# Kernel optimization log

Hardware: AMD Instinct MI355X
Metric: run time of the kernel (lower is better)

## Reference

```python
import jax, jax.numpy as jnp
import numpy as np

EPS = 1e-5
SLOPE = 0.2
K = 20
B, N = 8, 2048

def _lrelu(x):
    return jnp.where(x >= 0, x, SLOPE * x)

def _bn(x, g, b, m, v, axis):
    # eval-mode batchnorm with running stats
    shape = [1] * x.ndim
    shape[axis] = -1
    g, b, m, v = (t.reshape(shape) for t in (g, b, m, v))
    return g * (x - m) * jax.lax.rsqrt(v + EPS) + b

def _knn(x, k):
    # x: (B, C, N) -> neighbor indices (B, N, k) by largest negative sq dist
    xx = jnp.sum(x * x, axis=1)                      # (B, N)
    inner = jnp.einsum('bcn,bcm->bnm', x, x)         # (B, N, N)
    pd = 2.0 * inner - xx[:, :, None] - xx[:, None, :]
    return jax.lax.top_k(pd, k)[1]

def _graph_feature(x, k):
    # x: (B, C, N) -> (B, 2C, N, k) edge features [nbr - center, center]
    idx = _knn(x, k)                                  # (B, N, k)
    xt = jnp.transpose(x, (0, 2, 1))                  # (B, N, C)
    nbr = xt[jnp.arange(x.shape[0])[:, None, None], idx]  # (B, N, k, C)
    center = xt[:, :, None, :]
    f = jnp.concatenate([nbr - center, jnp.broadcast_to(center, nbr.shape)], axis=-1)
    return jnp.transpose(f, (0, 3, 1, 2))

def _edge_block(x, W, g, b, m, v):
    f = _graph_feature(x, K)                          # (B, 2C, N, k)
    h = jnp.einsum('oc,bcnk->bonk', W, f)             # 1x1 conv
    return jnp.max(_lrelu(_bn(h, g, b, m, v, 1)), axis=-1)

def _forward(x, W1, bn1_g, bn1_b, bn1_m, bn1_v, W2, bn2_g, bn2_b, bn2_m, bn2_v, W3, bn3_g, bn3_b, bn3_m, bn3_v, W4, bn4_g, bn4_b, bn4_m, bn4_v, l1_w, l1_b, bn5_g, bn5_b, bn5_m, bn5_v, l2_w, l2_b, bn6_g, bn6_b, bn6_m, bn6_v, l3_w, l3_b):
    xc = jnp.transpose(x, (0, 2, 1))                  # (B, 3, N)
    x1 = _edge_block(xc, W1, bn1_g, bn1_b, bn1_m, bn1_v)   # (B, 64, N)
    x2 = _edge_block(x1, W2, bn2_g, bn2_b, bn2_m, bn2_v)   # (B, 64, N)
    x3 = _edge_block(x2, W3, bn3_g, bn3_b, bn3_m, bn3_v)   # (B, 128, N)
    h = jnp.concatenate([x1, x2, x3], axis=1)         # (B, 256, N)
    h = _lrelu(_bn(jnp.einsum('oc,bcn->bon', W4, h), bn4_g, bn4_b, bn4_m, bn4_v, 1))
    h = jnp.max(h, axis=-1)                           # (B, 1024)
    h = _lrelu(_bn(h @ l1_w.T + l1_b, bn5_g, bn5_b, bn5_m, bn5_v, 1))
    h = _lrelu(_bn(h @ l2_w.T + l2_b, bn6_g, bn6_b, bn6_m, bn6_v, 1))
    return h @ l3_w.T + l3_b                          # (B, 2)

def setup_inputs() -> dict:
    key = jax.random.key(0)
    ks = iter(jax.random.split(key, 64))
    def rn(shape, s=1.0):
        return jax.random.normal(next(ks), shape, jnp.float32) * s
    def add_bn(inp, prefix, c):
        inp[prefix + '_g'] = jax.random.uniform(next(ks), (c,), jnp.float32, 0.5, 1.5)
        inp[prefix + '_b'] = rn((c,), 0.1)
        inp[prefix + '_m'] = rn((c,), 0.1)
        inp[prefix + '_v'] = jax.random.uniform(next(ks), (c,), jnp.float32, 0.5, 1.5)
    inp = {'x': rn((B, N, 3))}
    inp['W1'] = rn((64, 6), 0.3); add_bn(inp, 'bn1', 64)
    inp['W2'] = rn((64, 128), 0.1); add_bn(inp, 'bn2', 64)
    inp['W3'] = rn((128, 128), 0.1); add_bn(inp, 'bn3', 128)
    inp['W4'] = rn((1024, 256), 0.08); add_bn(inp, 'bn4', 1024)
    inp['l1_w'] = rn((512, 1024), 0.03); inp['l1_b'] = rn((512,), 0.01); add_bn(inp, 'bn5', 512)
    inp['l2_w'] = rn((256, 512), 0.05); inp['l2_b'] = rn((256,), 0.01); add_bn(inp, 'bn6', 256)
    inp['l3_w'] = rn((2, 256), 0.06); inp['l3_b'] = rn((2,), 0.01)
    return inp

def reference(x, W1, bn1_g, bn1_b, bn1_m, bn1_v, W2, bn2_g, bn2_b, bn2_m, bn2_v, W3, bn3_g, bn3_b, bn3_m, bn3_v, W4, bn4_g, bn4_b, bn4_m, bn4_v, l1_w, l1_b, bn5_g, bn5_b, bn5_m, bn5_v, l2_w, l2_b, bn6_g, bn6_b, bn6_m, bn6_v, l3_w, l3_b):
    return _forward(x, W1, bn1_g, bn1_b, bn1_m, bn1_v, W2, bn2_g, bn2_b, bn2_m, bn2_v, W3, bn3_g, bn3_b, bn3_m, bn3_v, W4, bn4_g, bn4_b, bn4_m, bn4_v, l1_w, l1_b, bn5_g, bn5_b, bn5_m, bn5_v, l2_w, l2_b, bn6_g, bn6_b, bn6_m, bn6_v, l3_w, l3_b)
```

## Files before the change

kernel.cpp:

```cpp
#include <hip/hip_runtime.h>
#include <math.h>

#define NN 2048
#define KK 20
#define EPSF 1e-5f

__device__ __forceinline__ float lrelu(float v){ return v >= 0.f ? v : 0.2f*v; }

__device__ __forceinline__ void topk20_insert(float d, int idc, float (&v)[KK], int (&id)[KK]){
#pragma unroll
  for (int j = KK-1; j >= 1; --j){
    bool cjm1 = d > v[j-1];
    bool cj   = d > v[j];
    float nv = cjm1 ? v[j-1] : (cj ? d   : v[j]);
    int   ni = cjm1 ? id[j-1] : (cj ? idc : id[j]);
    v[j] = nv; id[j] = ni;
  }
  if (d > v[0]) { v[0] = d; id[0] = idc; }
}

__global__ void k_prep1(const float* __restrict__ x, const float* __restrict__ W1,
                        float* __restrict__ Y, float* __restrict__ T, float* __restrict__ SQ){
  __shared__ float wa[64][3], wd[64][3];
  int t = threadIdx.x;
  if (t < 64){
#pragma unroll
    for (int c=0;c<3;c++){
      float a = W1[t*6+c], b2 = W1[t*6+3+c];
      wa[t][c] = a; wd[t][c] = b2 - a;
    }
  }
  __syncthreads();
  int gid = blockIdx.x*256 + t;
  int b = gid >> 11, n = gid & (NN-1);
  float px = x[gid*3+0], py = x[gid*3+1], pz = x[gid*3+2];
  SQ[gid] = px*px + py*py + pz*pz;
  float* yb = Y + ((size_t)b*128)*NN + n;
  float* tb = T + ((size_t)b*128)*NN + n;
#pragma unroll 8
  for (int o=0;o<64;o++){
    yb[(size_t)o*NN] = wa[o][0]*px + wa[o][1]*py + wa[o][2]*pz;
    tb[(size_t)o*NN] = wd[o][0]*px + wd[o][1]*py + wd[o][2]*pz;
  }
}

__global__ __launch_bounds__(256) void k_knn3(const float* __restrict__ x, const float* __restrict__ SQ,
                                              int* __restrict__ IDX){
  __shared__ __align__(16) unsigned char smem[30720];
  float* cd = (float*)smem;
  float* VL = (float*)smem;
  unsigned short* IL = (unsigned short*)(smem + 20480);
  int t = threadIdx.x;
  int b = blockIdx.x >> 6;
  int n_base = (blockIdx.x & 63) * 32;
  int ql = t & 31, sp = t >> 5;
  int n = n_base + ql;
  int gq = b*NN + n;
  float qx = x[gq*3], qy = x[gq*3+1], qz = x[gq*3+2];
  float qs = SQ[gq];
  float v[KK]; int id[KK];
#pragma unroll
  for (int i=0;i<KK;i++){ v[i] = -INFINITY; id[i] = 0; }
  int mlo = sp * 16;
  for (int tile=0; tile<16; ++tile){
    int m0 = tile * 128;
    __syncthreads();
#pragma unroll
    for (int i=0;i<2;i++){
      int f2 = t + i*256;
      int m = f2 >> 2, ch = f2 & 3;
      int gm = b*NN + m0 + m;
      cd[f2] = (ch < 3) ? x[gm*3 + ch] : SQ[gm];
    }
    __syncthreads();
    for (int j=mlo; j<mlo+16; ++j){
      float4 c4 = *(const float4*)&cd[j*4];
      float d = 2.f*(qx*c4.x + qy*c4.y + qz*c4.z) - qs - c4.w;
      if (d > v[KK-1]) topk20_insert(d, m0 + j, v, id);
    }
  }
  __syncthreads();
#pragma unroll
  for (int k2=0;k2<KK;k2++){
    VL[(ql*8+sp)*KK + k2] = v[k2];
    IL[(ql*8+sp)*KK + k2] = (unsigned short)id[k2];
  }
  __syncthreads();
  if (t < 32){
    float hv[8]; int hi_[8]; int hp[8];
#pragma unroll
    for (int s=0;s<8;s++){ hp[s]=0; hv[s]=VL[(t*8+s)*KK]; hi_[s]=(int)IL[(t*8+s)*KK]; }
    int nq = n_base + t;
    for (int r=0;r<KK;r++){
      float bv = hv[0]; int bi = hi_[0]; int bs = 0;
#pragma unroll
      for (int s=1;s<8;s++){
        bool win = (hv[s] > bv) || ((hv[s] == bv) && (hi_[s] < bi));
        bv = win ? hv[s] : bv; bi = win ? hi_[s] : bi; bs = win ? s : bs;
      }
      IDX[((size_t)b*KK + r)*NN + nq] = bi;
#pragma unroll
      for (int s=0;s<8;s++){
        if (s == bs){
          int np = hp[s] + 1; hp[s] = np;
          bool ok = np < KK;
          hv[s]  = ok ? VL[(t*8+s)*KK + np] : -INFINITY;
          hi_[s] = ok ? (int)IL[(t*8+s)*KK + np] : 0x7FFFFFFF;
        }
      }
    }
  }
}

__global__ void k_sqnorm(const float* __restrict__ X, float* __restrict__ SQ){
  int gid = blockIdx.x*256 + threadIdx.x;
  int b = gid >> 11, n = gid & (NN-1);
  const float* xb = X + (size_t)b*256*NN;
  float s = 0.f;
#pragma unroll
  for (int c=0;c<64;c++){ float vv = xb[(size_t)c*NN + n]; s += vv*vv; }
  SQ[gid] = s;
}

__global__ __launch_bounds__(256) void k_knn64(const float* __restrict__ X, const float* __restrict__ SQ,
                                               int* __restrict__ IDX){
  __shared__ __align__(16) unsigned char smem[35328];
  float* cd = (float*)smem;
  float* cs = (float*)(smem + 34816);
  float* VL = (float*)smem;
  unsigned short* IL = (unsigned short*)(smem + 20480);
  int t = threadIdx.x;
  int b = blockIdx.x >> 6;
  int n_base = (blockIdx.x & 63) * 32;
  int ql = t & 31, sp = t >> 5;
  int n = n_base + ql;
  const float* xb = X + (size_t)b*256*NN;
  float q[64];
#pragma unroll
  for (int c=0;c<64;c++) q[c] = xb[(size_t)c*NN + n];
  float qs = SQ[b*NN + n];
  float v[KK]; int id[KK];
#pragma unroll
  for (int i=0;i<KK;i++){ v[i]=-INFINITY; id[i]=0; }
  int mlo = sp * 16;
  for (int tile=0; tile<16; ++tile){
    int m0 = tile*128;
    __syncthreads();
#pragma unroll
    for (int i=0;i<32;i++){
      int flat = i*256 + t;
      int c = flat >> 7, m = flat & 127;
      cd[m*68 + c] = xb[(size_t)c*NN + m0 + m];
    }
    if (t < 128) cs[t] = SQ[b*NN + m0 + t];
    __syncthreads();
    for (int j=mlo; j<mlo+16; ++j){
      const float* crow = cd + j*68;
      float d = 0.f;
#pragma unroll
      for (int c=0;c<64;c+=4){
        float4 c4 = *(const float4*)&crow[c];
        d += q[c]*c4.x + q[c+1]*c4.y + q[c+2]*c4.z + q[c+3]*c4.w;
      }
      d = 2.f*d - qs - cs[j];
      if (d > v[KK-1]) topk20_insert(d, m0 + j, v, id);
    }
  }
  __syncthreads();
#pragma unroll
  for (int k2=0;k2<KK;k2++){
    VL[(ql*8+sp)*KK + k2] = v[k2];
    IL[(ql*8+sp)*KK + k2] = (unsigned short)id[k2];
  }
  __syncthreads();
  if (t < 32){
    float hv[8]; int hi_[8]; int hp[8];
#pragma unroll
    for (int s=0;s<8;s++){ hp[s]=0; hv[s]=VL[(t*8+s)*KK]; hi_[s]=(int)IL[(t*8+s)*KK]; }
    int nq = n_base + t;
    for (int r=0;r<KK;r++){
      float bv = hv[0]; int bi = hi_[0]; int bs = 0;
#pragma unroll
      for (int s=1;s<8;s++){
        bool win = (hv[s] > bv) || ((hv[s] == bv) && (hi_[s] < bi));
        bv = win ? hv[s] : bv; bi = win ? hi_[s] : bi; bs = win ? s : bs;
      }
      IDX[((size_t)b*KK + r)*NN + nq] = bi;
#pragma unroll
      for (int s=0;s<8;s++){
        if (s == bs){
          int np = hp[s] + 1; hp[s] = np;
          bool ok = np < KK;
          hv[s]  = ok ? VL[(t*8+s)*KK + np] : -INFINITY;
          hi_[s] = ok ? (int)IL[(t*8+s)*KK + np] : 0x7FFFFFFF;
        }
      }
    }
  }
}

__global__ __launch_bounds__(256) void k_edge_apply(const float* __restrict__ Y, const float* __restrict__ T,
                             const int* __restrict__ IDX,
                             const float* __restrict__ g, const float* __restrict__ be,
                             const float* __restrict__ mu, const float* __restrict__ va,
                             float* __restrict__ OUT, int c_off){
  int t = threadIdx.x;
  int nl = t & 127, oh = t >> 7;
  int n = blockIdx.x*128 + nl;
  int b = blockIdx.z;
  int o0 = blockIdx.y*32 + oh*16;
  int idx[KK];
#pragma unroll
  for (int k2=0;k2<KK;k2++) idx[k2] = IDX[((size_t)b*KK + k2)*NN + n];
  for (int oo=0;oo<16;oo++){
    int o = o0 + oo;
    const float* yrow = Y + ((size_t)b*128 + o)*NN;
    float M = -INFINITY;
#pragma unroll
    for (int k2=0;k2<KK;k2++) M = fmaxf(M, yrow[idx[k2]]);
    float s = g[o] * rsqrtf(va[o] + EPSF);
    float val = s*(M + T[((size_t)b*128 + o)*NN + n] - mu[o]) + be[o];
    OUT[((size_t)b*256 + c_off + o)*NN + n] = lrelu(val);
  }
}

template<int O>
__global__ __launch_bounds__(256) void k_yt_gemm(const float* __restrict__ X, const float* __restrict__ W,
                                                 float* __restrict__ Y, float* __restrict__ T){
  __shared__ __align__(16) float wa[O][64];
  __shared__ __align__(16) float wd[O][64];
  int t = threadIdx.x;
  for (int i=t; i<O*64; i+=256){
    int o = i >> 6, c = i & 63;
    float a = W[o*128 + c];
    wa[o][c] = a;
    wd[o][c] = W[o*128 + 64 + c] - a;
  }
  __syncthreads();
  int half = t >> 7, ln = t & 127;
  int gid = blockIdx.x*128 + ln;
  int b = gid >> 11, n = gid & (NN-1);
  const float* xb = X + (size_t)b*256*NN;
  float q[64];
#pragma unroll
  for (int c=0;c<64;c++) q[c] = xb[(size_t)c*NN + n];
  int o0 = half * (O/2);
  for (int o=o0; o<o0+O/2; ++o){
    float ay=0.f, at=0.f;
#pragma unroll
    for (int c=0;c<64;c+=4){
      float4 a4 = *(const float4*)&wa[o][c];
      float4 d4 = *(const float4*)&wd[o][c];
      ay += a4.x*q[c] + a4.y*q[c+1] + a4.z*q[c+2] + a4.w*q[c+3];
      at += d4.x*q[c] + d4.y*q[c+1] + d4.z*q[c+2] + d4.w*q[c+3];
    }
    Y[((size_t)b*128 + o)*NN + n] = ay;
    T[((size_t)b*128 + o)*NN + n] = at;
  }
}

__global__ __launch_bounds__(256) void k_w4max(const float* __restrict__ CAT, const float* __restrict__ W4,
                                               float* __restrict__ PART){
  __shared__ __align__(16) float wt[64][68];
  __shared__ __align__(16) float ct[64][68];
  int t = threadIdx.x;
  int io = t >> 4, in_ = t & 15;
  int nb = blockIdx.x * 64, ob = blockIdx.y * 64, b = blockIdx.z;
  const float* catb = CAT + (size_t)b*256*NN;
  float acc[4][4];
#pragma unroll
  for (int r=0;r<4;r++)
#pragma unroll
    for (int c=0;c<4;c++) acc[r][c]=0.f;
  for (int c0=0; c0<256; c0+=64){
    __syncthreads();
    for (int i=t; i<4096; i+=256){
      int oo = i >> 6, cc = i & 63;
      wt[cc][oo] = W4[(size_t)(ob+oo)*256 + c0 + cc];
    }
    for (int i=t; i<4096; i+=256){
      int cc = i >> 6, nn2 = i & 63;
      ct[cc][nn2] = catb[(size_t)(c0+cc)*NN + nb + nn2];
    }
    __syncthreads();
#pragma unroll 4
    for (int c=0;c<64;c++){
      float4 wv = *(const float4*)&wt[c][io*4];
      float4 cv = *(const float4*)&ct[c][in_*4];
      acc[0][0] += wv.x*cv.x; acc[0][1] += wv.x*cv.y; acc[0][2] += wv.x*cv.z; acc[0][3] += wv.x*cv.w;
      acc[1][0] += wv.y*cv.x; acc[1][1] += wv.y*cv.y; acc[1][2] += wv.y*cv.z; acc[1][3] += wv.y*cv.w;
      acc[2][0] += wv.z*cv.x; acc[2][1] += wv.z*cv.y; acc[2][2] += wv.z*cv.z; acc[2][3] += wv.z*cv.w;
      acc[3][0] += wv.w*cv.x; acc[3][1] += wv.w*cv.y; acc[3][2] += wv.w*cv.z; acc[3][3] += wv.w*cv.w;
    }
  }
#pragma unroll
  for (int r=0;r<4;r++){
    float m = fmaxf(fmaxf(acc[r][0], acc[r][1]), fmaxf(acc[r][2], acc[r][3]));
    m = fmaxf(m, __shfl_xor(m, 1));
    m = fmaxf(m, __shfl_xor(m, 2));
    m = fmaxf(m, __shfl_xor(m, 4));
    m = fmaxf(m, __shfl_xor(m, 8));
    if (in_ == 0){
      int o = ob + io*4 + r;
      PART[((size_t)b*1024 + o)*32 + blockIdx.x] = m;
    }
  }
}

__global__ void k_reduce4(const float* __restrict__ PART,
                          const float* __restrict__ g, const float* __restrict__ be,
                          const float* __restrict__ mu, const float* __restrict__ va,
                          float* __restrict__ H4){
  int gid = blockIdx.x*256 + threadIdx.x;
  int o = gid & 1023;
  float M = -INFINITY;
#pragma unroll
  for (int i=0;i<32;i++) M = fmaxf(M, PART[(size_t)gid*32 + i]);
  float s = g[o]*rsqrtf(va[o]+EPSF);
  H4[gid] = lrelu(s*(M - mu[o]) + be[o]);
}

__global__ __launch_bounds__(256) void k_mlp(const float* __restrict__ H4,
      const float* __restrict__ l1w, const float* __restrict__ l1b,
      const float* __restrict__ g5, const float* __restrict__ b5,
      const float* __restrict__ m5, const float* __restrict__ v5,
      const float* __restrict__ l2w, const float* __restrict__ l2b,
      const float* __restrict__ g6, const float* __restrict__ b6,
      const float* __restrict__ m6, const float* __restrict__ v6,
      const float* __restrict__ l3w, const float* __restrict__ l3b,
      float* __restrict__ out){
  __shared__ float h[1024];
  __shared__ float h5[512];
  __shared__ float h6[256];
  int b = blockIdx.x, t = threadIdx.x;
  for (int i=t;i<1024;i+=256) h[i] = H4[b*1024+i];
  __syncthreads();
  for (int o=t;o<512;o+=256){
    float acc = l1b[o];
    for (int c=0;c<1024;c+=4){
      float4 w = *(const float4*)&l1w[(size_t)o*1024 + c];
      acc += w.x*h[c] + w.y*h[c+1] + w.z*h[c+2] + w.w*h[c+3];
    }
    float s = g5[o]*rsqrtf(v5[o]+EPSF);
    h5[o] = lrelu(s*(acc - m5[o]) + b5[o]);
  }
  __syncthreads();
  if (t < 256){
    int o = t;
    float acc = l2b[o];
    for (int c=0;c<512;c+=4){
      float4 w = *(const float4*)&l2w[(size_t)o*512 + c];
      acc += w.x*h5[c] + w.y*h5[c+1] + w.z*h5[c+2] + w.w*h5[c+3];
    }
    float s = g6[o]*rsqrtf(v6[o]+EPSF);
    h6[o] = lrelu(s*(acc - m6[o]) + b6[o]);
  }
  __syncthreads();
  if (t < 128){
    int o = t >> 6, l = t & 63;
    float p = 0.f;
#pragma unroll
    for (int j=0;j<4;j++){ int c = j*64 + l; p += l3w[o*256 + c]*h6[c]; }
    p += __shfl_xor(p, 32); p += __shfl_xor(p, 16); p += __shfl_xor(p, 8);
    p += __shfl_xor(p, 4);  p += __shfl_xor(p, 2);  p += __shfl_xor(p, 1);
    if (l == 0) out[b*2 + o] = p + l3b[o];
  }
}

extern "C" void kernel_launch(void* const* d_in, const int* in_sizes, int n_in,
                              void* d_out, int out_size, void* d_ws, size_t ws_size,
                              hipStream_t stream){
  (void)in_sizes; (void)n_in; (void)out_size; (void)ws_size;
  const float* x    = (const float*)d_in[0];
  const float* W1   = (const float*)d_in[1];
  const float* bn1g = (const float*)d_in[2];
  const float* bn1b = (const float*)d_in[3];
  const float* bn1m = (const float*)d_in[4];
  const float* bn1v = (const float*)d_in[5];
  const float* W2   = (const float*)d_in[6];
  const float* bn2g = (const float*)d_in[7];
  const float* bn2b = (const float*)d_in[8];
  const float* bn2m = (const float*)d_in[9];
  const float* bn2v = (const float*)d_in[10];
  const float* W3   = (const float*)d_in[11];
  const float* bn3g = (const float*)d_in[12];
  const float* bn3b = (const float*)d_in[13];
  const float* bn3m = (const float*)d_in[14];
  const float* bn3v = (const float*)d_in[15];
  const float* W4   = (const float*)d_in[16];
  const float* bn4g = (const float*)d_in[17];
  const float* bn4b = (const float*)d_in[18];
  const float* bn4m = (const float*)d_in[19];
  const float* bn4v = (const float*)d_in[20];
  const float* l1w  = (const float*)d_in[21];
  const float* l1b  = (const float*)d_in[22];
  const float* bn5g = (const float*)d_in[23];
  const float* bn5b = (const float*)d_in[24];
  const float* bn5m = (const float*)d_in[25];
  const float* bn5v = (const float*)d_in[26];
  const float* l2w  = (const float*)d_in[27];
  const float* l2b  = (const float*)d_in[28];
  const float* bn6g = (const float*)d_in[29];
  const float* bn6b = (const float*)d_in[30];
  const float* bn6m = (const float*)d_in[31];
  const float* bn6v = (const float*)d_in[32];
  const float* l3w  = (const float*)d_in[33];
  const float* l3b  = (const float*)d_in[34];

  float* CAT  = (float*)d_ws;
  float* Yb   = CAT + (size_t)8*256*NN;
  float* Tb   = Yb  + (size_t)8*128*NN;
  float* SQ   = Tb  + (size_t)8*128*NN;
  int*   IDX  = (int*)(SQ + (size_t)8*NN);
  float* PART = (float*)(IDX + (size_t)8*KK*NN);
  float* H4   = PART + (size_t)8*1024*32;

  k_prep1<<<64,256,0,stream>>>(x, W1, Yb, Tb, SQ);
  k_knn3<<<512,256,0,stream>>>(x, SQ, IDX);
  k_edge_apply<<<dim3(16,2,8),256,0,stream>>>(Yb, Tb, IDX, bn1g, bn1b, bn1m, bn1v, CAT, 0);
  k_sqnorm<<<64,256,0,stream>>>(CAT, SQ);
  k_knn64<<<512,256,0,stream>>>(CAT, SQ, IDX);
  k_yt_gemm<64><<<128,256,0,stream>>>(CAT, W2, Yb, Tb);
  k_edge_apply<<<dim3(16,2,8),256,0,stream>>>(Yb, Tb, IDX, bn2g, bn2b, bn2m, bn2v, CAT, 64);
  k_sqnorm<<<64,256,0,stream>>>(CAT + (size_t)64*NN, SQ);
  k_knn64<<<512,256,0,stream>>>(CAT + (size_t)64*NN, SQ, IDX);
  k_yt_gemm<128><<<128,256,0,stream>>>(CAT + (size_t)64*NN, W3, Yb, Tb);
  k_edge_apply<<<dim3(16,4,8),256,0,stream>>>(Yb, Tb, IDX, bn3g, bn3b, bn3m, bn3v, CAT, 128);
  k_w4max<<<dim3(32,16,8),256,0,stream>>>(CAT, W4, PART);
  k_reduce4<<<32,256,0,stream>>>(PART, bn4g, bn4b, bn4m, bn4v, H4);
  k_mlp<<<8,256,0,stream>>>(H4, l1w, l1b, bn5g, bn5b, bn5m, bn5v,
                            l2w, l2b, bn6g, bn6b, bn6m, bn6v, l3w, l3b, (float*)d_out);
}
```

Measured before the change: 1.501 ms.

## Split kNN candidate range across blocks with merge; retile W4 GEMM-max to 128x128

The kNN kernels now split the 2048 candidates into two halves handled by separate blocks, which doubles the grid from 512 to 1024 blocks. Each half writes a partial sorted top-20 of values and indices, and a new merge kernel combines them. Separately, W4 is transposed once into a workspace, and the W4·CAT max kernel moves from 64x64 tiles with 4x4 per-thread outputs to 128x128 tiles with 8x8 outputs and float4 loads, halving the partial-max count. The costs are extra partial-buffer traffic, three merge launches, a transpose launch and higher register pressure in the GEMM.

```diff
diff --git a/kernel.cpp b/kernel.cpp
--- a/kernel.cpp
+++ b/kernel.cpp
@@ -44,15 +44,18 @@
   }
 }
 
-__global__ __launch_bounds__(256) void k_knn3(const float* __restrict__ x, const float* __restrict__ SQ,
-                                              int* __restrict__ IDX){
+__global__ __launch_bounds__(256) void k_knn3_part(const float* __restrict__ x, const float* __restrict__ SQ,
+                                                   float* __restrict__ PV, unsigned short* __restrict__ PI){
   __shared__ __align__(16) unsigned char smem[30720];
   float* cd = (float*)smem;
   float* VL = (float*)smem;
   unsigned short* IL = (unsigned short*)(smem + 20480);
   int t = threadIdx.x;
-  int b = blockIdx.x >> 6;
-  int n_base = (blockIdx.x & 63) * 32;
+  int bx = blockIdx.x;
+  int cs = bx & 1, nb = bx >> 1;
+  int b = blockIdx.y;
+  int n_base = nb * 32;
+  int cbase = cs * 1024;
   int ql = t & 31, sp = t >> 5;
   int n = n_base + ql;
   int gq = b*NN + n;
@@ -62,8 +65,8 @@
 #pragma unroll
   for (int i=0;i<KK;i++){ v[i] = -INFINITY; id[i] = 0; }
   int mlo = sp * 16;
-  for (int tile=0; tile<16; ++tile){
-    int m0 = tile * 128;
+  for (int tile=0; tile<8; ++tile){
+    int m0 = cbase + tile * 128;
     __syncthreads();
 #pragma unroll
     for (int i=0;i<2;i++){
@@ -98,7 +101,8 @@
         bool win = (hv[s] > bv) || ((hv[s] == bv) && (hi_[s] < bi));
         bv = win ? hv[s] : bv; bi = win ? hi_[s] : bi; bs = win ? s : bs;
       }
-      IDX[((size_t)b*KK + r)*NN + nq] = bi;
+      PV[(((size_t)b*2 + cs)*KK + r)*NN + nq] = bv;
+      PI[(((size_t)b*2 + cs)*KK + r)*NN + nq] = (unsigned short)bi;
 #pragma unroll
       for (int s=0;s<8;s++){
         if (s == bs){
@@ -122,16 +126,19 @@
   SQ[gid] = s;
 }
 
-__global__ __launch_bounds__(256) void k_knn64(const float* __restrict__ X, const float* __restrict__ SQ,
-                                               int* __restrict__ IDX){
+__global__ __launch_bounds__(256) void k_knn64_part(const float* __restrict__ X, const float* __restrict__ SQ,
+                                                    float* __restrict__ PV, unsigned short* __restrict__ PI){
   __shared__ __align__(16) unsigned char smem[35328];
   float* cd = (float*)smem;
-  float* cs = (float*)(smem + 34816);
+  float* cs_ = (float*)(smem + 34816);
   float* VL = (float*)smem;
   unsigned short* IL = (unsigned short*)(smem + 20480);
   int t = threadIdx.x;
-  int b = blockIdx.x >> 6;
-  int n_base = (blockIdx.x & 63) * 32;
+  int bx = blockIdx.x;
+  int cs = bx & 1, nb = bx >> 1;
+  int b = blockIdx.y;
+  int n_base = nb * 32;
+  int cbase = cs * 1024;
   int ql = t & 31, sp = t >> 5;
   int n = n_base + ql;
   const float* xb = X + (size_t)b*256*NN;
@@ -143,8 +150,8 @@
 #pragma unroll
   for (int i=0;i<KK;i++){ v[i]=-INFINITY; id[i]=0; }
   int mlo = sp * 16;
-  for (int tile=0; tile<16; ++tile){
-    int m0 = tile*128;
+  for (int tile=0; tile<8; ++tile){
+    int m0 = cbase + tile*128;
     __syncthreads();
 #pragma unroll
     for (int i=0;i<32;i++){
@@ -152,7 +159,7 @@
       int c = flat >> 7, m = flat & 127;
       cd[m*68 + c] = xb[(size_t)c*NN + m0 + m];
     }
-    if (t < 128) cs[t] = SQ[b*NN + m0 + t];
+    if (t < 128) cs_[t] = SQ[b*NN + m0 + t];
     __syncthreads();
     for (int j=mlo; j<mlo+16; ++j){
       const float* crow = cd + j*68;
@@ -162,7 +169,7 @@
         float4 c4 = *(const float4*)&crow[c];
         d += q[c]*c4.x + q[c+1]*c4.y + q[c+2]*c4.z + q[c+3]*c4.w;
       }
-      d = 2.f*d - qs - cs[j];
+      d = 2.f*d - qs - cs_[j];
       if (d > v[KK-1]) topk20_insert(d, m0 + j, v, id);
     }
   }
@@ -185,7 +192,8 @@
         bool win = (hv[s] > bv) || ((hv[s] == bv) && (hi_[s] < bi));
         bv = win ? hv[s] : bv; bi = win ? hi_[s] : bi; bs = win ? s : bs;
       }
-      IDX[((size_t)b*KK + r)*NN + nq] = bi;
+      PV[(((size_t)b*2 + cs)*KK + r)*NN + nq] = bv;
+      PI[(((size_t)b*2 + cs)*KK + r)*NN + nq] = (unsigned short)bi;
 #pragma unroll
       for (int s=0;s<8;s++){
         if (s == bs){
@@ -199,6 +207,28 @@
   }
 }
 
+__global__ void k_topk_merge(const float* __restrict__ PV, const unsigned short* __restrict__ PI,
+                             int* __restrict__ IDX){
+  int gid = blockIdx.x*256 + threadIdx.x;
+  int b = gid >> 11, n = gid & (NN-1);
+  float av[KK], bv[KK]; int ai[KK], bi[KK];
+#pragma unroll
+  for (int k=0;k<KK;k++){
+    av[k] = PV[(((size_t)b*2+0)*KK + k)*NN + n];
+    ai[k] = (int)PI[(((size_t)b*2+0)*KK + k)*NN + n];
+    bv[k] = PV[(((size_t)b*2+1)*KK + k)*NN + n];
+    bi[k] = (int)PI[(((size_t)b*2+1)*KK + k)*NN + n];
+  }
+  int p0=0, p1=0;
+  for (int r=0;r<KK;r++){
+    float a = av[p0], bb = bv[p1];
+    int ia = ai[p0], ib = bi[p1];
+    bool w1 = (bb > a) || ((bb == a) && (ib < ia));
+    IDX[((size_t)b*KK + r)*NN + n] = w1 ? ib : ia;
+    if (w1) ++p1; else ++p0;
+  }
+}
+
 __global__ __launch_bounds__(256) void k_edge_apply(const float* __restrict__ Y, const float* __restrict__ T,
                              const int* __restrict__ IDX,
                              const float* __restrict__ g, const float* __restrict__ be,
@@ -259,50 +289,79 @@
   }
 }
 
-__global__ __launch_bounds__(256) void k_w4max(const float* __restrict__ CAT, const float* __restrict__ W4,
+__global__ __launch_bounds__(256) void k_w4t(const float* __restrict__ W4, float* __restrict__ W4T){
+  __shared__ float Tt[64][65];
+  int t = threadIdx.x;
+  int c0 = blockIdx.x * 64, o0 = blockIdx.y * 64;
+#pragma unroll
+  for (int p=0;p<16;p++){
+    int f = p*256 + t;
+    int i = f >> 6, j = f & 63;
+    Tt[i][j] = W4[(size_t)(o0+i)*256 + c0 + j];
+  }
+  __syncthreads();
+#pragma unroll
+  for (int p=0;p<16;p++){
+    int f = p*256 + t;
+    int i = f >> 6, j = f & 63;
+    W4T[(size_t)(c0+i)*1024 + o0 + j] = Tt[j][i];
+  }
+}
+
+__global__ __launch_bounds__(256) void k_w4max(const float* __restrict__ CAT, const float* __restrict__ W4T,
                                                float* __restrict__ PART){
-  __shared__ __align__(16) float wt[64][68];
-  __shared__ __align__(16) float ct[64][68];
+  __shared__ __align__(16) float wt[32][132];
+  __shared__ __align__(16) float ct[32][132];
   int t = threadIdx.x;
   int io = t >> 4, in_ = t & 15;
-  int nb = blockIdx.x * 64, ob = blockIdx.y * 64, b = blockIdx.z;
+  int nb = blockIdx.x * 128, ob = blockIdx.y * 128, b = blockIdx.z;
   const float* catb = CAT + (size_t)b*256*NN;
-  float acc[4][4];
-#pragma unroll
-  for (int r=0;r<4;r++)
-#pragma unroll
-    for (int c=0;c<4;c++) acc[r][c]=0.f;
-  for (int c0=0; c0<256; c0+=64){
-    __syncthreads();
-    for (int i=t; i<4096; i+=256){
-      int oo = i >> 6, cc = i & 63;
-      wt[cc][oo] = W4[(size_t)(ob+oo)*256 + c0 + cc];
-    }
-    for (int i=t; i<4096; i+=256){
-      int cc = i >> 6, nn2 = i & 63;
-      ct[cc][nn2] = catb[(size_t)(c0+cc)*NN + nb + nn2];
+  float acc[8][8];
+#pragma unroll
+  for (int r=0;r<8;r++)
+#pragma unroll
+    for (int c=0;c<8;c++) acc[r][c]=0.f;
+  for (int c0=0; c0<256; c0+=32){
+    __syncthreads();
+#pragma unroll
+    for (int p=0;p<4;p++){
+      int idx = p*256 + t;
+      int cc = idx >> 5, o4 = (idx & 31) * 4;
+      *(float4*)&wt[cc][o4] = *(const float4*)&W4T[(size_t)(c0+cc)*1024 + ob + o4];
+    }
+#pragma unroll
+    for (int p=0;p<4;p++){
+      int idx = p*256 + t;
+      int cc = idx >> 5, n4 = (idx & 31) * 4;
+      *(float4*)&ct[cc][n4] = *(const float4*)&catb[(size_t)(c0+cc)*NN + nb + n4];
     }
     __syncthreads();
 #pragma unroll 4
-    for (int c=0;c<64;c++){
-      float4 wv = *(const float4*)&wt[c][io*4];
-      float4 cv = *(const float4*)&ct[c][in_*4];
-      acc[0][0] += wv.x*cv.x; acc[0][1] += wv.x*cv.y; acc[0][2] += wv.x*cv.z; acc[0][3] += wv.x*cv.w;
-      acc[1][0] += wv.y*cv.x; acc[1][1] += wv.y*cv.y; acc[1][2] += wv.y*cv.z; acc[1][3] += wv.y*cv.w;
-      acc[2][0] += wv.z*cv.x; acc[2][1] += wv.z*cv.y; acc[2][2] += wv.z*cv.z; acc[2][3] += wv.z*cv.w;
-      acc[3][0] += wv.w*cv.x; acc[3][1] += wv.w*cv.y; acc[3][2] += wv.w*cv.z; acc[3][3] += wv.w*cv.w;
-    }
-  }
-#pragma unroll
-  for (int r=0;r<4;r++){
-    float m = fmaxf(fmaxf(acc[r][0], acc[r][1]), fmaxf(acc[r][2], acc[r][3]));
+    for (int c=0;c<32;c++){
+      float4 a0 = *(const float4*)&wt[c][io*8];
+      float4 a1 = *(const float4*)&wt[c][io*8+4];
+      float4 b0 = *(const float4*)&ct[c][in_*8];
+      float4 b1 = *(const float4*)&ct[c][in_*8+4];
+      float ar[8] = {a0.x,a0.y,a0.z,a0.w,a1.x,a1.y,a1.z,a1.w};
+      float br[8] = {b0.x,b0.y,b0.z,b0.w,b1.x,b1.y,b1.z,b1.w};
+#pragma unroll
+      for (int r=0;r<8;r++)
+#pragma unroll
+        for (int s=0;s<8;s++) acc[r][s] += ar[r]*br[s];
+    }
+  }
+#pragma unroll
+  for (int r=0;r<8;r++){
+    float m = acc[r][0];
+#pragma unroll
+    for (int s=1;s<8;s++) m = fmaxf(m, acc[r][s]);
     m = fmaxf(m, __shfl_xor(m, 1));
     m = fmaxf(m, __shfl_xor(m, 2));
     m = fmaxf(m, __shfl_xor(m, 4));
     m = fmaxf(m, __shfl_xor(m, 8));
     if (in_ == 0){
-      int o = ob + io*4 + r;
-      PART[((size_t)b*1024 + o)*32 + blockIdx.x] = m;
+      int o = ob + io*8 + r;
+      PART[((size_t)b*1024 + o)*16 + blockIdx.x] = m;
     }
   }
 }
@@ -315,7 +374,7 @@
   int o = gid & 1023;
   float M = -INFINITY;
 #pragma unroll
-  for (int i=0;i<32;i++) M = fmaxf(M, PART[(size_t)gid*32 + i]);
+  for (int i=0;i<16;i++) M = fmaxf(M, PART[(size_t)gid*16 + i]);
   float s = g[o]*rsqrtf(va[o]+EPSF);
   H4[gid] = lrelu(s*(M - mu[o]) + be[o]);
 }
@@ -413,20 +472,27 @@
   float* SQ   = Tb  + (size_t)8*128*NN;
   int*   IDX  = (int*)(SQ + (size_t)8*NN);
   float* PART = (float*)(IDX + (size_t)8*KK*NN);
-  float* H4   = PART + (size_t)8*1024*32;
-
+  float* H4   = PART + (size_t)8*1024*16;
+  float* W4T  = H4 + (size_t)8*1024;
+  float* PTV  = W4T + (size_t)256*1024;
+  unsigned short* PTI = (unsigned short*)(PTV + (size_t)8*2*KK*NN);
+
+  k_w4t<<<dim3(4,16),256,0,stream>>>(W4, W4T);
   k_prep1<<<64,256,0,stream>>>(x, W1, Yb, Tb, SQ);
-  k_knn3<<<512,256,0,stream>>>(x, SQ, IDX);
+  k_knn3_part<<<dim3(128,8),256,0,stream>>>(x, SQ, PTV, PTI);
+  k_topk_merge<<<64,256,0,stream>>>(PTV, PTI, IDX);
   k_edge_apply<<<dim3(16,2,8),256,0,stream>>>(Yb, Tb, IDX, bn1g, bn1b, bn1m, bn1v, CAT, 0);
   k_sqnorm<<<64,256,0,stream>>>(CAT, SQ);
-  k_knn64<<<512,256,0,stream>>>(CAT, SQ, IDX);
+  k_knn64_part<<<dim3(128,8),256,0,stream>>>(CAT, SQ, PTV, PTI);
+  k_topk_merge<<<64,256,0,stream>>>(PTV, PTI, IDX);
   k_yt_gemm<64><<<128,256,0,stream>>>(CAT, W2, Yb, Tb);
   k_edge_apply<<<dim3(16,2,8),256,0,stream>>>(Yb, Tb, IDX, bn2g, bn2b, bn2m, bn2v, CAT, 64);
   k_sqnorm<<<64,256,0,stream>>>(CAT + (size_t)64*NN, SQ);
-  k_knn64<<<512,256,0,stream>>>(CAT + (size_t)64*NN, SQ, IDX);
+  k_knn64_part<<<dim3(128,8),256,0,stream>>>(CAT + (size_t)64*NN, SQ, PTV, PTI);
+  k_topk_merge<<<64,256,0,stream>>>(PTV, PTI, IDX);
   k_yt_gemm<128><<<128,256,0,stream>>>(CAT + (size_t)64*NN, W3, Yb, Tb);
   k_edge_apply<<<dim3(16,4,8),256,0,stream>>>(Yb, Tb, IDX, bn3g, bn3b, bn3m, bn3v, CAT, 128);
-  k_w4max<<<dim3(32,16,8),256,0,stream>>>(CAT, W4, PART);
+  k_w4max<<<dim3(16,8,8),256,0,stream>>>(CAT, W4T, PART);
   k_reduce4<<<32,256,0,stream>>>(PART, bn4g, bn4b, bn4m, bn4v, H4);
   k_mlp<<<8,256,0,stream>>>(H4, l1w, l1b, bn5g, bn5b, bn5m, bn5v,
                             l2w, l2b, bn6g, bn6b, bn6m, bn6v, l3w, l3b, (float*)d_out);
```

Measured after the change: 1.506 ms. About the same (+0.3%).
